# Kernel optimization log

Hardware: AMD Instinct MI355X
Metric: run time of the kernel (lower is better)

Reference implementation:

```python
import jax, jax.numpy as jnp
import numpy as np

NUM_HEADS = 4
GROUPS = 16
EPS = 1e-5


def setup_inputs() -> dict:
    key = jax.random.key(0)
    ks = jax.random.split(key, 7)
    b, c, hh, ww = 4, 256, 64, 64
    x = jax.random.normal(ks[0], (b, c, hh, ww), dtype=jnp.float32)
    norm_w = 1.0 + 0.1 * jax.random.normal(ks[1], (c,), dtype=jnp.float32)
    norm_b = 0.1 * jax.random.normal(ks[2], (c,), dtype=jnp.float32)
    qkv_w = jax.random.normal(ks[3], (3 * c, c), dtype=jnp.float32) / np.sqrt(c)
    qkv_b = 0.01 * jax.random.normal(ks[4], (3 * c,), dtype=jnp.float32)
    # NOTE: original zero-inits proj_out; we use random weights so the
    # attention path actually affects the output (kernel correctness test).
    proj_w = jax.random.normal(ks[5], (c, c), dtype=jnp.float32) / np.sqrt(c)
    proj_b = jnp.zeros((c,), dtype=jnp.float32)
    return {"x": x, "norm_w": norm_w, "norm_b": norm_b,
            "qkv_w": qkv_w, "qkv_b": qkv_b,
            "proj_w": proj_w, "proj_b": proj_b}


def _group_norm(x, w, b):
    # x: [B, C, T]; GroupNorm32 computes in fp32 (inputs already fp32)
    B, C, T = x.shape
    xg = x.reshape(B, GROUPS, C // GROUPS, T)
    mean = jnp.mean(xg, axis=(2, 3), keepdims=True)
    var = jnp.var(xg, axis=(2, 3), keepdims=True)
    xn = ((xg - mean) * jax.lax.rsqrt(var + EPS)).reshape(B, C, T)
    return xn * w[None, :, None] + b[None, :, None]


def reference(x, norm_w, norm_b, qkv_w, qkv_b, proj_w, proj_b):
    b, c = x.shape[0], x.shape[1]
    spatial = x.shape[2:]
    x2 = x.reshape(b, c, -1)                       # [B, C, T]
    T = x2.shape[-1]
    normed = _group_norm(x2, norm_w, norm_b)
    qkv = jnp.einsum('oc,bct->bot', qkv_w, normed) + qkv_b[None, :, None]
    # faithful reshape: [B, 3C, T] -> [B*H, 3C/H, T], then split in thirds
    qkv = qkv.reshape(b * NUM_HEADS, (3 * c) // NUM_HEADS, T)
    ch = qkv.shape[1] // 3                         # = C / H
    q, k, v = jnp.split(qkv, 3, axis=1)
    scale = 1.0 / np.sqrt(np.sqrt(ch))
    weight = jnp.einsum('bct,bcs->bts', q * scale, k * scale)
    weight = jax.nn.softmax(weight.astype(jnp.float32), axis=-1).astype(qkv.dtype)
    h = jnp.einsum('bts,bcs->bct', weight, v)      # [B*H, ch, T]
    h = h.reshape(b, c, T)
    h = jnp.einsum('oc,bct->bot', proj_w, h) + proj_b[None, :, None]
    return (x2 + h).reshape(b, c, *spatial)
```

## Files before the change

### kernel.cpp

```cpp
#include <hip/hip_runtime.h>

constexpr int kB  = 4;
constexpr int kC  = 256;
constexpr int kT  = 4096;
constexpr int kG  = 16;
constexpr int kCg = kC / kG;
constexpr int kH  = 4;
constexpr int kCh = kC / kH;
constexpr float kEps = 1e-5f;
constexpr float kQScale = 0.125f * 1.4426950408889634f;

typedef short bf16x8 __attribute__((ext_vector_type(8)));
typedef float f32x4  __attribute__((ext_vector_type(4)));
typedef float f32x16 __attribute__((ext_vector_type(16)));

__device__ inline unsigned short f2bf(float f) {
    union { float f; unsigned u; } v; v.f = f;
    unsigned r = v.u + 0x7fffu + ((v.u >> 16) & 1u);
    return (unsigned short)(r >> 16);
}
__device__ inline unsigned pk2bf(float a, float b) {
    return (unsigned)f2bf(a) | ((unsigned)f2bf(b) << 16);
}
__device__ inline unsigned pk2bf_trunc(float a, float b) {
    return __builtin_amdgcn_perm(__float_as_uint(b), __float_as_uint(a), 0x07060302u);
}

__global__ __launch_bounds__(256) void prep_kernel(const float* __restrict__ x,
                                                   float* __restrict__ stats,
                                                   const float* __restrict__ qkv_w,
                                                   const float* __restrict__ proj_w,
                                                   unsigned short* __restrict__ wbf) {
    int tid = threadIdx.x;
    if (blockIdx.x >= 64) {
        int gid = (blockIdx.x - 64) * 256 + tid;
        for (int i = gid; i < 65536; i += 128 * 256) {
            float4 v = (i < 49152) ? ((const float4*)qkv_w)[i]
                                   : ((const float4*)proj_w)[i - 49152];
            *(uint2*)&wbf[(size_t)i * 4] = make_uint2(pk2bf(v.x, v.y), pk2bf(v.z, v.w));
        }
        return;
    }
    int bg = blockIdx.x;
    const float4* xp4 = (const float4*)(x + (size_t)bg * (kCg * kT));
    float s = 0.f, q = 0.f;
    #pragma unroll 4
    for (int i = 0; i < (kCg * kT / 4) / 256; ++i) {
        float4 v = xp4[tid + i * 256];
        s += v.x + v.y + v.z + v.w;
        q += v.x * v.x + v.y * v.y + v.z * v.z + v.w * v.w;
    }
    #pragma unroll
    for (int off = 32; off > 0; off >>= 1) {
        s += __shfl_down(s, off);
        q += __shfl_down(q, off);
    }
    __shared__ float rs[4], rq[4];
    int wid = tid >> 6, lane = tid & 63;
    if (lane == 0) { rs[wid] = s; rq[wid] = q; }
    __syncthreads();
    if (tid == 0) {
        float S = rs[0] + rs[1] + rs[2] + rs[3];
        float Q = rq[0] + rq[1] + rq[2] + rq[3];
        const float invN = 1.0f / (float)(kCg * kT);
        float mean = S * invN;
        float var  = Q * invN - mean * mean;
        stats[bg * 2 + 0] = mean;
        stats[bg * 2 + 1] = rsqrtf(var + kEps);
    }
}

__global__ __launch_bounds__(256) void gn_apply_t_kernel(const float* __restrict__ x,
                                                         const float* __restrict__ stats,
                                                         const float* __restrict__ w,
                                                         const float* __restrict__ bias,
                                                         unsigned short* __restrict__ normT) {
    __shared__ float Ls[64][65];
    int t0 = blockIdx.x * 64;
    int c0 = blockIdx.y * 64;
    int b  = blockIdx.z;
    int tid = threadIdx.x;
    #pragma unroll
    for (int p = 0; p < 4; ++p) {
        int idx = tid + p * 256;
        int cl = idx >> 4, t4 = idx & 15;
        int c = c0 + cl;
        int bg = b * kG + (c >> 4);
        float mean = stats[bg * 2 + 0];
        float rstd = stats[bg * 2 + 1];
        float sw = w[c] * rstd;
        float sb = bias[c] - mean * sw;
        float4 v = *(const float4*)&x[((size_t)b * kC + c) * kT + t0 + t4 * 4];
        Ls[t4 * 4 + 0][cl] = v.x * sw + sb;
        Ls[t4 * 4 + 1][cl] = v.y * sw + sb;
        Ls[t4 * 4 + 2][cl] = v.z * sw + sb;
        Ls[t4 * 4 + 3][cl] = v.w * sw + sb;
    }
    __syncthreads();
    {
        int row = tid >> 2, cq = (tid & 3) * 16;
        unsigned tmp[8];
        #pragma unroll
        for (int i = 0; i < 8; ++i)
            tmp[i] = pk2bf(Ls[row][cq + 2 * i], Ls[row][cq + 2 * i + 1]);
        uint4* dst = (uint4*)&normT[((size_t)b * kT + t0 + row) * kC + c0 + cq];
        dst[0] = make_uint4(tmp[0], tmp[1], tmp[2], tmp[3]);
        dst[1] = make_uint4(tmp[4], tmp[5], tmp[6], tmp[7]);
    }
}

__global__ __launch_bounds__(256) void qkv_gemm_kernel(const unsigned short* __restrict__ wbf,
                                                       const float* __restrict__ qkv_b,
                                                       const unsigned short* __restrict__ normT,
                                                       unsigned short* __restrict__ qTg,
                                                       unsigned short* __restrict__ kTg,
                                                       unsigned short* __restrict__ vCg) {
    constexpr int LDK = 72;
    constexpr int LDV = 136;
    __shared__ __align__(16) unsigned short As[64 * LDK];
    __shared__ __align__(16) unsigned short Bs[128 * LDK];

    int t0 = blockIdx.x * 128;
    int m0 = blockIdx.y * 64;
    int b  = blockIdx.z;
    const unsigned short* Ab = wbf + (size_t)m0 * kC;
    const unsigned short* Bb = normT + (size_t)b * kT * kC;

    int tid = threadIdx.x;
    int wave = tid >> 6, lane = tid & 63;
    int ln15 = lane & 15, quad = lane >> 4;
    int wm = wave >> 1, wt = wave & 1;

    f32x4 acc[2][4] = {};

    for (int k0 = 0; k0 < kC; k0 += 64) {
        __syncthreads();
        #pragma unroll
        for (int p = 0; p < 2; ++p) {
            int idx = tid + p * 256;
            int row = idx >> 3, seg = idx & 7;
            *(uint4*)&As[row * LDK + seg * 8] =
                *(const uint4*)&Ab[(size_t)row * kC + k0 + seg * 8];
        }
        #pragma unroll
        for (int p = 0; p < 4; ++p) {
            int idx = tid + p * 256;
            int row = idx >> 3, seg = idx & 7;
            *(uint4*)&Bs[row * LDK + seg * 8] =
                *(const uint4*)&Bb[(size_t)(t0 + row) * kC + k0 + seg * 8];
        }
        __syncthreads();
        #pragma unroll
        for (int ks = 0; ks < 2; ++ks) {
            bf16x8 af[2], bf[4];
            #pragma unroll
            for (int i = 0; i < 2; ++i)
                af[i] = *(bf16x8*)&As[(wm * 32 + i * 16 + ln15) * LDK + ks * 32 + quad * 8];
            #pragma unroll
            for (int j = 0; j < 4; ++j)
                bf[j] = *(bf16x8*)&Bs[(wt * 64 + j * 16 + ln15) * LDK + ks * 32 + quad * 8];
            #pragma unroll
            for (int i = 0; i < 2; ++i)
                #pragma unroll
                for (int j = 0; j < 4; ++j)
                    acc[i][j] = __builtin_amdgcn_mfma_f32_16x16x32_bf16(
                        af[i], bf[j], acc[i][j], 0, 0, 0);
        }
    }

    int type = (m0 % 192) / 64;
    int h = m0 / 192;
    int bh = b * kH + h;
    __syncthreads();
    #pragma unroll
    for (int i = 0; i < 2; ++i) {
        float4 bv = *(const float4*)&qkv_b[m0 + wm * 32 + i * 16 + quad * 4];
        const float* bp = (const float*)&bv;
        #pragma unroll
        for (int j = 0; j < 4; ++j) {
            int tl = wt * 64 + j * 16 + ln15;
            int c = wm * 32 + i * 16 + quad * 4;
            float v0 = acc[i][j][0] + bp[0];
            float v1 = acc[i][j][1] + bp[1];
            float v2 = acc[i][j][2] + bp[2];
            float v3 = acc[i][j][3] + bp[3];
            if (type == 0) {
                v0 *= kQScale; v1 *= kQScale; v2 *= kQScale; v3 *= kQScale;
            }
            if (type != 2) {
                *(uint2*)&Bs[tl * LDK + c] = make_uint2(pk2bf(v0, v1), pk2bf(v2, v3));
            } else {
                Bs[(c + 0) * LDV + tl] = f2bf(v0);
                Bs[(c + 1) * LDV + tl] = f2bf(v1);
                Bs[(c + 2) * LDV + tl] = f2bf(v2);
                Bs[(c + 3) * LDV + tl] = f2bf(v3);
            }
        }
    }
    __syncthreads();
    if (type != 2) {
        unsigned short* base = ((type == 0) ? qTg : kTg) + (size_t)bh * (kT * kCh);
        #pragma unroll
        for (int p = 0; p < 4; ++p) {
            int f = tid + p * 256;
            int ln = f & 31, hif = (f >> 5) & 1, ks = (f >> 6) & 3, tb = f >> 8;
            *(uint4*)&base[((t0 >> 5) + tb) * 2048 + ks * 512 + hif * 256 + ln * 8] =
                *(uint4*)&Bs[(tb * 32 + ln) * LDK + ks * 16 + hif * 8];
        }
    } else {
        unsigned short* base = vCg + (size_t)bh * (kT * kCh);
        #pragma unroll
        for (int p = 0; p < 4; ++p) {
            int f = tid + p * 256;
            int c = f & 63, hif = (f >> 6) & 1, sg = f >> 7;
            *(uint4*)&base[((t0 >> 4) + sg) * 1024 + hif * 512 + c * 8] =
                *(uint4*)&Bs[c * LDV + sg * 16 + hif * 8];
        }
    }
}

__global__ __launch_bounds__(256, 2) void attn_mfma_kernel(const unsigned short* __restrict__ qTg,
                                                           const unsigned short* __restrict__ kTg,
                                                           const unsigned short* __restrict__ vCg,
                                                           unsigned short* __restrict__ attnT) {
    constexpr int LDPu = 36;
    __shared__ __align__(16) unsigned int Ps[4][32 * LDPu];

    int bh = blockIdx.y;
    int t0 = blockIdx.x * 128;
    int b = bh >> 2, h = bh & 3;

    int tid = threadIdx.x;
    int wave = tid >> 6, lane = tid & 63;
    int ln31 = lane & 31, hi = lane >> 5;
    unsigned int* Pw = &Ps[wave][0];

    const unsigned short* qb = qTg + (size_t)bh * (kT * kCh);
    const unsigned short* kb = kTg + (size_t)bh * (kT * kCh);
    const unsigned short* vb = vCg + (size_t)bh * (kT * kCh);

    bf16x8 qf[4];
    {
        const unsigned short* qp = qb + ((t0 >> 5) + wave) * 2048 + hi * 256 + ln31 * 8;
        #pragma unroll
        for (int ks = 0; ks < 4; ++ks) qf[ks] = *(const bf16x8*)(qp + ks * 512);
    }
    const unsigned short* kptr = kb + hi * 256 + ln31 * 8;
    const unsigned short* vptr = vb + hi * 512 + ln31 * 8;

    bf16x8 kf[8], vf[8];
    #pragma unroll
    for (int i = 0; i < 8; ++i)
        kf[i] = *(const bf16x8*)(kptr + (i >> 2) * 2048 + (i & 3) * 512);
    #pragma unroll
    for (int i = 0; i < 8; ++i)
        vf[i] = *(const bf16x8*)(vptr + (i & 3) * 1024 + (i >> 2) * 256);

    float l_r = 0.f;
    f32x16 accO0 = {}, accO1 = {};
    union PunP { uint4 u; bf16x8 f; };

    for (int s0 = 0; s0 < kT; s0 += 64) {
        f32x16 accS0 = {}, accS1 = {};
        #pragma unroll
        for (int ks = 0; ks < 4; ++ks)
            accS0 = __builtin_amdgcn_mfma_f32_32x32x16_bf16(kf[ks], qf[ks], accS0, 0, 0, 0);
        #pragma unroll
        for (int ks = 0; ks < 4; ++ks)
            accS1 = __builtin_amdgcn_mfma_f32_32x32x16_bf16(kf[4 + ks], qf[ks], accS1, 0, 0, 0);

        if (s0 + 64 < kT) {
            kptr += 4096;
            #pragma unroll
            for (int i = 0; i < 8; ++i)
                kf[i] = *(const bf16x8*)(kptr + (i >> 2) * 2048 + (i & 3) * 512);
        }

        float rs = 0.f;
        #pragma unroll
        for (int g = 0; g < 4; ++g) {
            float p0 = __builtin_amdgcn_exp2f(accS0[4 * g + 0]);
            float p1 = __builtin_amdgcn_exp2f(accS0[4 * g + 1]);
            float p2 = __builtin_amdgcn_exp2f(accS0[4 * g + 2]);
            float p3 = __builtin_amdgcn_exp2f(accS0[4 * g + 3]);
            rs += (p0 + p1) + (p2 + p3);
            int ui = ln31 * LDPu + 4 * g + 2 * hi;
            Pw[ui + 0] = pk2bf_trunc(p0, p1);
            Pw[ui + 1] = pk2bf_trunc(p2, p3);
        }
        #pragma unroll
        for (int g = 0; g < 4; ++g) {
            float p0 = __builtin_amdgcn_exp2f(accS1[4 * g + 0]);
            float p1 = __builtin_amdgcn_exp2f(accS1[4 * g + 1]);
            float p2 = __builtin_amdgcn_exp2f(accS1[4 * g + 2]);
            float p3 = __builtin_amdgcn_exp2f(accS1[4 * g + 3]);
            rs += (p0 + p1) + (p2 + p3);
            int ui = ln31 * LDPu + 16 + 4 * g + 2 * hi;
            Pw[ui + 0] = pk2bf_trunc(p0, p1);
            Pw[ui + 1] = pk2bf_trunc(p2, p3);
        }
        rs += __shfl_xor(rs, 32);
        l_r += rs;
        __asm__ __volatile__("" ::: "memory");

        #pragma unroll
        for (int i = 0; i < 4; ++i) {
            PunP pk;
            pk.u = *(const uint4*)&Pw[ln31 * LDPu + i * 8 + hi * 4];
            accO0 = __builtin_amdgcn_mfma_f32_32x32x16_bf16(vf[i],     pk.f, accO0, 0, 0, 0);
            accO1 = __builtin_amdgcn_mfma_f32_32x32x16_bf16(vf[4 + i], pk.f, accO1, 0, 0, 0);
        }

        if (s0 + 64 < kT) {
            vptr += 4096;
            #pragma unroll
            for (int i = 0; i < 8; ++i)
                vf[i] = *(const bf16x8*)(vptr + (i & 3) * 1024 + (i >> 2) * 256);
        }
        __asm__ __volatile__("" ::: "memory");
    }

    float linv = 1.0f / l_r;
    int t = t0 + wave * 32 + ln31;
    #pragma unroll
    for (int ct = 0; ct < 2; ++ct) {
        const f32x16& ao = ct ? accO1 : accO0;
        #pragma unroll
        for (int g = 0; g < 4; ++g) {
            int c = h * kCh + ct * 32 + 8 * g + 4 * hi;
            float v0 = ao[4 * g + 0] * linv;
            float v1 = ao[4 * g + 1] * linv;
            float v2 = ao[4 * g + 2] * linv;
            float v3 = ao[4 * g + 3] * linv;
            *(uint2*)&attnT[((size_t)b * kT + t) * kC + c] =
                make_uint2(pk2bf(v0, v1), pk2bf(v2, v3));
        }
    }
}

__global__ __launch_bounds__(256) void proj_gemm_kernel(const unsigned short* __restrict__ wpbf,
                                                        const float* __restrict__ proj_b,
                                                        const unsigned short* __restrict__ attnT,
                                                        const float* __restrict__ x,
                                                        float* __restrict__ out) {
    constexpr int LDK = 72;
    __shared__ __align__(16) unsigned short As[64 * LDK];
    __shared__ __align__(16) unsigned short Bs[128 * LDK];

    int t0 = blockIdx.x * 128;
    int m0 = blockIdx.y * 64;
    int b  = blockIdx.z;
    const unsigned short* Ab = wpbf + (size_t)m0 * kC;
    const unsigned short* Bb = attnT + (size_t)b * kT * kC;

    int tid = threadIdx.x;
    int wave = tid >> 6, lane = tid & 63;
    int ln15 = lane & 15, quad = lane >> 4;
    int wm = wave >> 1, wt = wave & 1;

    f32x4 acc[2][4] = {};

    for (int k0 = 0; k0 < kC; k0 += 64) {
        __syncthreads();
        #pragma unroll
        for (int p = 0; p < 2; ++p) {
            int idx = tid + p * 256;
            int row = idx >> 3, seg = idx & 7;
            *(uint4*)&As[row * LDK + seg * 8] =
                *(const uint4*)&Ab[(size_t)row * kC + k0 + seg * 8];
        }
        #pragma unroll
        for (int p = 0; p < 4; ++p) {
            int idx = tid + p * 256;
            int row = idx >> 3, seg = idx & 7;
            *(uint4*)&Bs[row * LDK + seg * 8] =
                *(const uint4*)&Bb[(size_t)(t0 + row) * kC + k0 + seg * 8];
        }
        __syncthreads();
        #pragma unroll
        for (int ks = 0; ks < 2; ++ks) {
            bf16x8 af[2], bf[4];
            #pragma unroll
            for (int i = 0; i < 2; ++i)
                af[i] = *(bf16x8*)&As[(wm * 32 + i * 16 + ln15) * LDK + ks * 32 + quad * 8];
            #pragma unroll
            for (int j = 0; j < 4; ++j)
                bf[j] = *(bf16x8*)&Bs[(wt * 64 + j * 16 + ln15) * LDK + ks * 32 + quad * 8];
            #pragma unroll
            for (int i = 0; i < 2; ++i)
                #pragma unroll
                for (int j = 0; j < 4; ++j)
                    acc[i][j] = __builtin_amdgcn_mfma_f32_16x16x32_bf16(
                        af[i], bf[j], acc[i][j], 0, 0, 0);
        }
    }

    #pragma unroll
    for (int i = 0; i < 2; ++i) {
        float4 bv = *(const float4*)&proj_b[m0 + wm * 32 + i * 16 + quad * 4];
        const float* bp = (const float*)&bv;
        #pragma unroll
        for (int j = 0; j < 4; ++j) {
            int t = t0 + wt * 64 + j * 16 + ln15;
            int mbase = m0 + wm * 32 + i * 16 + quad * 4;
            #pragma unroll
            for (int r = 0; r < 4; ++r) {
                size_t off = ((size_t)b * kC + mbase + r) * kT + t;
                out[off] = acc[i][j][r] + bp[r] + x[off];
            }
        }
    }
}

extern "C" void kernel_launch(void* const* d_in, const int* in_sizes, int n_in,
                              void* d_out, int out_size, void* d_ws, size_t ws_size,
                              hipStream_t stream) {
    const float* x      = (const float*)d_in[0];
    const float* norm_w = (const float*)d_in[1];
    const float* norm_b = (const float*)d_in[2];
    const float* qkv_w  = (const float*)d_in[3];
    const float* qkv_b  = (const float*)d_in[4];
    const float* proj_w = (const float*)d_in[5];
    const float* proj_b = (const float*)d_in[6];
    float* out = (float*)d_out;

    float* stats = (float*)d_ws;
    unsigned short* wsbf  = (unsigned short*)((float*)d_ws + 128);
    unsigned short* normT = wsbf;
    unsigned short* wbf   = normT + (size_t)kB * kT * kC;
    unsigned short* qTp   = wbf + 262144;
    unsigned short* kTp   = qTp + (size_t)kB * kH * kT * kCh;
    unsigned short* vCp   = kTp + (size_t)kB * kH * kT * kCh;
    unsigned short* attnT = vCp + (size_t)kB * kH * kT * kCh;
    unsigned short* wpbf  = wbf + 196608;

    prep_kernel<<<192, 256, 0, stream>>>(x, stats, qkv_w, proj_w, wbf);
    gn_apply_t_kernel<<<dim3(kT / 64, kC / 64, kB), 256, 0, stream>>>(
        x, stats, norm_w, norm_b, normT);
    qkv_gemm_kernel<<<dim3(kT / 128, 12, kB), 256, 0, stream>>>(
        wbf, qkv_b, normT, qTp, kTp, vCp);
    attn_mfma_kernel<<<dim3(kT / 128, kB * kH), 256, 0, stream>>>(qTp, kTp, vCp, attnT);
    proj_gemm_kernel<<<dim3(kT / 128, kC / 64, kB), 256, 0, stream>>>(
        wpbf, proj_b, attnT, x, out);
}
```

Before: 215.7 us.

## Split attention over two key halves and combine partials in projection GEMM

The attention kernel now splits the key/value sequence into two halves along a new grid dimension. Each half writes unnormalized fp32 partial outputs and row sums, and the projection GEMM sums the two partials, normalizes and converts to bf16 while staging. This doubles the block count (from 512 to 1024) to fill the GPU better, and raises the occupancy hint from 2 to 4. The cost is larger fp32 intermediate traffic in both kernels and extra work in the GEMM load path. Merging without a running max relies on scores staying small enough that exp2 does not overflow, which the original kernel already assumed.

New measurement: 365.8 us. 1.7x slower.

```diff
diff --git a/kernel.cpp b/kernel.cpp
--- a/kernel.cpp
+++ b/kernel.cpp
@@ -219,15 +219,17 @@
     }
 }
 
-__global__ __launch_bounds__(256, 2) void attn_mfma_kernel(const unsigned short* __restrict__ qTg,
+__global__ __launch_bounds__(256, 4) void attn_mfma_kernel(const unsigned short* __restrict__ qTg,
                                                            const unsigned short* __restrict__ kTg,
                                                            const unsigned short* __restrict__ vCg,
-                                                           unsigned short* __restrict__ attnT) {
+                                                           float* __restrict__ oPart,
+                                                           float* __restrict__ lPart) {
     constexpr int LDPu = 36;
     __shared__ __align__(16) unsigned int Ps[4][32 * LDPu];
 
     int bh = blockIdx.y;
     int t0 = blockIdx.x * 128;
+    int sz = blockIdx.z;
     int b = bh >> 2, h = bh & 3;
 
     int tid = threadIdx.x;
@@ -245,8 +247,8 @@
         #pragma unroll
         for (int ks = 0; ks < 4; ++ks) qf[ks] = *(const bf16x8*)(qp + ks * 512);
     }
-    const unsigned short* kptr = kb + hi * 256 + ln31 * 8;
-    const unsigned short* vptr = vb + hi * 512 + ln31 * 8;
+    const unsigned short* kptr = kb + sz * 131072 + hi * 256 + ln31 * 8;
+    const unsigned short* vptr = vb + sz * 131072 + hi * 512 + ln31 * 8;
 
     bf16x8 kf[8], vf[8];
     #pragma unroll
@@ -260,7 +262,7 @@
     f32x16 accO0 = {}, accO1 = {};
     union PunP { uint4 u; bf16x8 f; };
 
-    for (int s0 = 0; s0 < kT; s0 += 64) {
+    for (int it = 0; it < 32; ++it) {
         f32x16 accS0 = {}, accS1 = {};
         #pragma unroll
         for (int ks = 0; ks < 4; ++ks)
@@ -269,7 +271,7 @@
         for (int ks = 0; ks < 4; ++ks)
             accS1 = __builtin_amdgcn_mfma_f32_32x32x16_bf16(kf[4 + ks], qf[ks], accS1, 0, 0, 0);
 
-        if (s0 + 64 < kT) {
+        if (it + 1 < 32) {
             kptr += 4096;
             #pragma unroll
             for (int i = 0; i < 8; ++i)
@@ -311,7 +313,7 @@
             accO1 = __builtin_amdgcn_mfma_f32_32x32x16_bf16(vf[4 + i], pk.f, accO1, 0, 0, 0);
         }
 
-        if (s0 + 64 < kT) {
+        if (it + 1 < 32) {
             vptr += 4096;
             #pragma unroll
             for (int i = 0; i < 8; ++i)
@@ -320,27 +322,26 @@
         __asm__ __volatile__("" ::: "memory");
     }
 
-    float linv = 1.0f / l_r;
     int t = t0 + wave * 32 + ln31;
+    float* op = oPart + ((size_t)sz * kB + b) * kT * kC;
     #pragma unroll
     for (int ct = 0; ct < 2; ++ct) {
         const f32x16& ao = ct ? accO1 : accO0;
         #pragma unroll
         for (int g = 0; g < 4; ++g) {
             int c = h * kCh + ct * 32 + 8 * g + 4 * hi;
-            float v0 = ao[4 * g + 0] * linv;
-            float v1 = ao[4 * g + 1] * linv;
-            float v2 = ao[4 * g + 2] * linv;
-            float v3 = ao[4 * g + 3] * linv;
-            *(uint2*)&attnT[((size_t)b * kT + t) * kC + c] =
-                make_uint2(pk2bf(v0, v1), pk2bf(v2, v3));
-        }
-    }
+            *(float4*)&op[(size_t)t * kC + c] =
+                make_float4(ao[4 * g + 0], ao[4 * g + 1], ao[4 * g + 2], ao[4 * g + 3]);
+        }
+    }
+    if (hi == 0)
+        lPart[((size_t)sz * (kB * kH) + bh) * kT + t] = l_r;
 }
 
 __global__ __launch_bounds__(256) void proj_gemm_kernel(const unsigned short* __restrict__ wpbf,
                                                         const float* __restrict__ proj_b,
-                                                        const unsigned short* __restrict__ attnT,
+                                                        const float* __restrict__ oPart,
+                                                        const float* __restrict__ lPart,
                                                         const float* __restrict__ x,
                                                         float* __restrict__ out) {
     constexpr int LDK = 72;
@@ -351,7 +352,8 @@
     int m0 = blockIdx.y * 64;
     int b  = blockIdx.z;
     const unsigned short* Ab = wpbf + (size_t)m0 * kC;
-    const unsigned short* Bb = attnT + (size_t)b * kT * kC;
+    const float* O0 = oPart + (size_t)b * kT * kC;
+    const float* O1 = oPart + ((size_t)kB + b) * kT * kC;
 
     int tid = threadIdx.x;
     int wave = tid >> 6, lane = tid & 63;
@@ -361,6 +363,9 @@
     f32x4 acc[2][4] = {};
 
     for (int k0 = 0; k0 < kC; k0 += 64) {
+        int h = k0 >> 6;
+        const float* l0p = lPart + ((size_t)b * kH + h) * kT;
+        const float* l1p = lPart + ((size_t)(kB * kH) + b * kH + h) * kT;
         __syncthreads();
         #pragma unroll
         for (int p = 0; p < 2; ++p) {
@@ -373,8 +378,18 @@
         for (int p = 0; p < 4; ++p) {
             int idx = tid + p * 256;
             int row = idx >> 3, seg = idx & 7;
-            *(uint4*)&Bs[row * LDK + seg * 8] =
-                *(const uint4*)&Bb[(size_t)(t0 + row) * kC + k0 + seg * 8];
+            int t = t0 + row;
+            size_t off = (size_t)t * kC + k0 + seg * 8;
+            float4 a0 = *(const float4*)&O0[off];
+            float4 b0 = *(const float4*)&O0[off + 4];
+            float4 a1 = *(const float4*)&O1[off];
+            float4 b1 = *(const float4*)&O1[off + 4];
+            float rl = 1.0f / (l0p[t] + l1p[t]);
+            unsigned u0 = pk2bf((a0.x + a1.x) * rl, (a0.y + a1.y) * rl);
+            unsigned u1 = pk2bf((a0.z + a1.z) * rl, (a0.w + a1.w) * rl);
+            unsigned u2 = pk2bf((b0.x + b1.x) * rl, (b0.y + b1.y) * rl);
+            unsigned u3 = pk2bf((b0.z + b1.z) * rl, (b0.w + b1.w) * rl);
+            *(uint4*)&Bs[row * LDK + seg * 8] = make_uint4(u0, u1, u2, u3);
         }
         __syncthreads();
         #pragma unroll
@@ -431,7 +446,8 @@
     unsigned short* qTp   = wbf + 262144;
     unsigned short* kTp   = qTp + (size_t)kB * kH * kT * kCh;
     unsigned short* vCp   = kTp + (size_t)kB * kH * kT * kCh;
-    unsigned short* attnT = vCp + (size_t)kB * kH * kT * kCh;
+    float* oPart = (float*)(vCp + (size_t)kB * kH * kT * kCh);
+    float* lPart = oPart + (size_t)2 * kB * kT * kC;
     unsigned short* wpbf  = wbf + 196608;
 
     prep_kernel<<<192, 256, 0, stream>>>(x, stats, qkv_w, proj_w, wbf);
@@ -439,7 +455,8 @@
         x, stats, norm_w, norm_b, normT);
     qkv_gemm_kernel<<<dim3(kT / 128, 12, kB), 256, 0, stream>>>(
         wbf, qkv_b, normT, qTp, kTp, vCp);
-    attn_mfma_kernel<<<dim3(kT / 128, kB * kH), 256, 0, stream>>>(qTp, kTp, vCp, attnT);
+    attn_mfma_kernel<<<dim3(kT / 128, kB * kH, 2), 256, 0, stream>>>(
+        qTp, kTp, vCp, oPart, lPart);
     proj_gemm_kernel<<<dim3(kT / 128, kC / 64, kB), 256, 0, stream>>>(
-        wpbf, proj_b, attnT, x, out);
-}
+        wpbf, proj_b, oPart, lPart, x, out);
+}
```
